# Kernel optimization log

Hardware: AMD Instinct MI355X
Metric: run time of the kernel (lower is better)

## Reference

```python
import jax, jax.numpy as jnp
import numpy as np

EPS = 1e-5

def ste_sign(x):
    # forward: sign(x) in {-1,+1}; backward: straight-through with |x|<=1 clip
    xc = jnp.clip(x, -1.0, 1.0)
    s = jnp.where(x >= 0, 1.0, -1.0).astype(x.dtype)
    return xc + jax.lax.stop_gradient(s - xc)

def quant_w(w):
    # 1-bit weight: sign(w) scaled by mean |w| (XNOR-Net style)
    return ste_sign(w) * jnp.mean(jnp.abs(w))

def qconv(x, w, stride, pad):
    # quantized conv: binarize activations and weights, then dense conv
    xq = ste_sign(x)
    wq = quant_w(w)
    return jax.lax.conv_general_dilated(
        xq, wq, window_strides=(stride, stride),
        padding=[(pad, pad), (pad, pad)],
        dimension_numbers=('NCHW', 'OIHW', 'NCHW'))

def batchnorm(x, gamma, beta):
    # training-mode BN: batch statistics over (N, H, W)
    mu = jnp.mean(x, axis=(0, 2, 3), keepdims=True)
    var = jnp.var(x, axis=(0, 2, 3), keepdims=True)
    xhat = (x - mu) * jax.lax.rsqrt(var + EPS)
    return xhat * gamma[None, :, None, None] + beta[None, :, None, None]

def setup_inputs() -> dict:
    key = jax.random.key(0)
    ks = jax.random.split(key, 4)
    in_planes, planes = 128, 256
    x = jax.random.normal(ks[0], (64, in_planes, 56, 56), dtype=jnp.float32)
    w1 = jax.random.normal(ks[1], (planes, in_planes, 3, 3), dtype=jnp.float32) * 0.05
    w2 = jax.random.normal(ks[2], (planes, planes, 3, 3), dtype=jnp.float32) * 0.05
    ws = jax.random.normal(ks[3], (planes, in_planes, 1, 1), dtype=jnp.float32) * 0.05
    g1 = jnp.ones((planes,), jnp.float32); b1 = jnp.zeros((planes,), jnp.float32)
    g2 = jnp.ones((planes,), jnp.float32); b2 = jnp.zeros((planes,), jnp.float32)
    return {'x': x, 'w1': w1, 'g1': g1, 'b1': b1, 'w2': w2, 'g2': g2, 'b2': b2, 'ws': ws}

def reference(x, w1, g1, b1, w2, g2, b2, ws):
    out = batchnorm(qconv(x, w1, stride=2, pad=1), g1, b1)   # [N,256,28,28]
    out = qconv(out, w2, stride=1, pad=1)
    out = out + qconv(x, ws, stride=2, pad=0)                # quantized 1x1 shortcut
    out = batchnorm(out, g2, b2)
    return out
```

## Files before the change

### kernel.cpp

```cpp
#include <hip/hip_runtime.h>
#include <stdint.h>

#define N_    64
#define CIN   128
#define CMID  256
#define H_    56
#define W_    56
#define OH    28
#define OW    28
#define NPIX  (OH*OW)
#define MPAD  800
#define MTOT  (N_*MPAD)
#define CNT_CH (N_*NPIX)
#define PXH   58
#define PYH   30
#define EPS_  1e-5f

#define STATS_BYTES 16384
#define OFF_PXI 16384
#define OFF_PYI (OFF_PXI + 27551744)
#define OFF_W1F (OFF_PYI + 14745600)
#define OFF_W2F (OFF_W1F + 294912)
#define OFF_WSF (OFF_W2F + 589824)
#define MEMSET_BYTES OFF_W1F

typedef int v4i  __attribute__((ext_vector_type(4)));
typedef int v16i __attribute__((ext_vector_type(16)));

#define MFMA_I8 __builtin_amdgcn_mfma_i32_32x32x32_i8

typedef const __attribute__((address_space(1))) void* gas_t;
typedef __attribute__((address_space(3))) void* las_t;

__device__ __forceinline__ void gl_lds16(const void* g, void* l) {
  __builtin_amdgcn_global_load_lds((gas_t)g, (las_t)l, 16, 0, 0);
}

__global__ __launch_bounds__(256) void reduce_abs_k(const float* __restrict__ w, int n,
                                                    float* __restrict__ out) {
  float s = 0.f;
  for (int i = blockIdx.x * 256 + threadIdx.x; i < n; i += gridDim.x * 256)
    s += fabsf(w[i]);
  for (int off = 32; off; off >>= 1) s += __shfl_down(s, off);
  if ((threadIdx.x & 63) == 0) atomicAdd(out, s);
}

__global__ __launch_bounds__(256) void pack_x_k(const float* __restrict__ x,
                                                int8_t* __restrict__ px) {
  int idx = blockIdx.x * 256 + threadIdx.x;
  int n = idx / (H_ * W_), hw = idx - n * (H_ * W_);
  int ih = hw / W_, iw = hw - ih * W_;
  const float* xp = x + ((size_t)n * CIN) * (H_ * W_) + hw;
  uint32_t wd[32];
#pragma unroll
  for (int c4 = 0; c4 < 32; ++c4) {
    uint32_t wv = 0u;
#pragma unroll
    for (int j = 0; j < 4; ++j) {
      uint32_t b = (xp[(size_t)(c4 * 4 + j) * (H_ * W_)] >= 0.f) ? 0x01u : 0xFFu;
      wv |= b << (j * 8);
    }
    wd[c4] = wv;
  }
  uint4* dst = (uint4*)(px + (((size_t)n * (PXH * PXH) + (ih + 1) * PXH + (iw + 1)) * CIN));
#pragma unroll
  for (int q = 0; q < 8; ++q)
    dst[q] = make_uint4(wd[q * 4], wd[q * 4 + 1], wd[q * 4 + 2], wd[q * 4 + 3]);
}

__global__ __launch_bounds__(256) void packw1f_k(const float* __restrict__ w1,
                                                 uint32_t* __restrict__ w1f) {
  int T = blockIdx.x * 256 + threadIdx.x;
  int l = T & 63, fb = T >> 6;
  int nb = fb & 7, kc = fb >> 3;
  int o = nb * 32 + (l & 31);
  int kbase = kc * 32 + (l >> 5) * 16;
  uint32_t wd[4] = {0u, 0u, 0u, 0u};
#pragma unroll
  for (int j = 0; j < 16; ++j) {
    int k = kbase + j, t = k >> 7, c = k & 127;
    uint32_t b = (w1[((size_t)o * CIN + c) * 9 + t] >= 0.f) ? 0x01u : 0xFFu;
    wd[j >> 2] |= b << ((j & 3) * 8);
  }
  ((uint4*)w1f)[T] = make_uint4(wd[0], wd[1], wd[2], wd[3]);
}

__global__ __launch_bounds__(256) void packw2f_k(const float* __restrict__ w2,
                                                 uint32_t* __restrict__ w2f) {
  int T = blockIdx.x * 256 + threadIdx.x;
  int l = T & 63, fb = T >> 6;
  int nb = fb & 7, kc = fb >> 3;
  int o = nb * 32 + (l & 31);
  int kbase = kc * 32 + (l >> 5) * 16;
  uint32_t wd[4] = {0u, 0u, 0u, 0u};
#pragma unroll
  for (int j = 0; j < 16; ++j) {
    int k = kbase + j, t = k >> 8, c = k & 255;
    uint32_t b = (w2[((size_t)o * CMID + c) * 9 + t] >= 0.f) ? 0x01u : 0xFFu;
    wd[j >> 2] |= b << ((j & 3) * 8);
  }
  ((uint4*)w2f)[T] = make_uint4(wd[0], wd[1], wd[2], wd[3]);
}

__global__ __launch_bounds__(256) void packwsf_k(const float* __restrict__ ws,
                                                 uint32_t* __restrict__ wsf) {
  int T = blockIdx.x * 256 + threadIdx.x;
  int l = T & 63, fb = T >> 6;
  int nb = fb & 7, kc = fb >> 3;
  int o = nb * 32 + (l & 31);
  int kbase = kc * 32 + (l >> 5) * 16;
  uint32_t wd[4] = {0u, 0u, 0u, 0u};
#pragma unroll
  for (int j = 0; j < 16; ++j) {
    int c = kbase + j;
    uint32_t b = (ws[(size_t)o * CIN + c] >= 0.f) ? 0x01u : 0xFFu;
    wd[j >> 2] |= b << ((j & 3) * 8);
  }
  ((uint4*)wsf)[T] = make_uint4(wd[0], wd[1], wd[2], wd[3]);
}

__global__ __launch_bounds__(256, 2) void conv1_k(const int8_t* __restrict__ px,
                                                  const uint8_t* __restrict__ w1f,
                                                  short* __restrict__ y16,
                                                  float* __restrict__ stats) {
  __shared__ int8_t lds[2][32768];
  int bid = (blockIdx.x & 7) * 100 + (blockIdx.x >> 3);
  int bnh = bid & 1, bm = bid >> 1;
  int tid = threadIdx.x, w = tid >> 6, l = tid & 63;
  int l31 = l & 31, lhi = l >> 5;
  int blockM = bm * 128;
  int waveM = blockM + (w & 1) * 64;
  int waveN = bnh * 128 + (w >> 1) * 64;
  int nbgl2 = (w >> 1) * 2;

  int srcsw = (((l & 7) ^ (l >> 3)) << 4);
  uint32_t rowoff[4];
#pragma unroll
  for (int i = 0; i < 4; ++i) {
    int p = blockM + (w * 4 + i) * 8 + (l >> 3);
    int n = p / MPAD, hw = p - n * MPAD;
    if (hw >= NPIX) hw = 0;
    int oh = hw / OW, ow = hw - oh * OW;
    rowoff[i] = (uint32_t)((n * (PXH * PXH) + (2 * oh) * PXH + 2 * ow) * CIN);
  }
  int sw = (l31 & 7) << 4;
  uint32_t aoff[2][4];
#pragma unroll
  for (int m = 0; m < 2; ++m) {
    int pxl = (w & 1) * 64 + m * 32 + l31;
#pragma unroll
    for (int kcl = 0; kcl < 4; ++kcl)
      aoff[m][kcl] = (uint32_t)(pxl * 128 + ((kcl * 32 + lhi * 16) ^ sw));
  }

  v16i acc[2][2] = {};

  auto stage = [&](int t, int8_t* buf) {
    int kh = t / 3, kw = t - 3 * kh;
    uint32_t tapoff = (uint32_t)((kh * PXH + kw) * CIN);
#pragma unroll
    for (int i = 0; i < 4; ++i) {
      int ch = w * 4 + i;
      gl_lds16(px + (size_t)(rowoff[i] + tapoff) + srcsw, buf + ch * 1024);
      gl_lds16(w1f + ((size_t)(((t * 4 + w) * 8) + bnh * 4 + i) << 10) + l * 16,
               buf + 16384 + ch * 1024);
    }
  };

  stage(0, lds[0]);
  __syncthreads();
  for (int it = 0; it < 9; ++it) {
    if (it < 8) stage(it + 1, lds[(it + 1) & 1]);
    const int8_t* cbuf = lds[it & 1];
    v4i a[2][4], b[2][4];
#pragma unroll
    for (int m = 0; m < 2; ++m)
#pragma unroll
      for (int kcl = 0; kcl < 4; ++kcl)
        a[m][kcl] = *(const v4i*)(cbuf + aoff[m][kcl]);
#pragma unroll
    for (int n2 = 0; n2 < 2; ++n2)
#pragma unroll
      for (int kcl = 0; kcl < 4; ++kcl)
        b[n2][kcl] = *(const v4i*)(cbuf + 16384 + (kcl * 4 + nbgl2 + n2) * 1024 + l * 16);
#pragma unroll
    for (int kcl = 0; kcl < 4; ++kcl) {
      acc[0][0] = MFMA_I8(a[0][kcl], b[0][kcl], acc[0][0], 0, 0, 0);
      acc[0][1] = MFMA_I8(a[0][kcl], b[1][kcl], acc[0][1], 0, 0, 0);
      acc[1][0] = MFMA_I8(a[1][kcl], b[0][kcl], acc[1][0], 0, 0, 0);
      acc[1][1] = MFMA_I8(a[1][kcl], b[1][kcl], acc[1][1], 0, 0, 0);
    }
    __syncthreads();
  }

#pragma unroll
  for (int n2 = 0; n2 < 2; ++n2) {
    int o = waveN + n2 * 32 + l31;
    float ssum = 0.f, ssq = 0.f;
#pragma unroll
    for (int m = 0; m < 2; ++m) {
      int tbase = waveM + m * 32;
      int nb0 = tbase / MPAD, r0 = tbase - nb0 * MPAD;
#pragma unroll
      for (int r = 0; r < 16; ++r) {
        int row = (r & 3) + 8 * (r >> 2) + 4 * lhi;
        int hwr = r0 + row;
        int d = acc[m][n2][r];
        bool valid = hwr < NPIX;
        if (valid) y16[((size_t)nb0 * NPIX + hwr) * CMID + o] = (short)d;
        float fd = valid ? (float)d : 0.f;
        ssum += fd; ssq += fd * fd;
      }
    }
    ssum += __shfl_down(ssum, 32);
    ssq  += __shfl_down(ssq, 32);
    if (l < 32) { atomicAdd(&stats[16 + o], ssum); atomicAdd(&stats[272 + o], ssq); }
  }
}

__global__ void bn1_prep_k(float* __restrict__ stats,
                           const float* __restrict__ g1,
                           const float* __restrict__ b1) {
  int c = threadIdx.x;
  float alpha1 = stats[0] * (1.f / (CMID * CIN * 9));
  float S = stats[16 + c], S2 = stats[272 + c];
  float mu = alpha1 * (S * (1.f / CNT_CH));
  float ey2 = alpha1 * alpha1 * (S2 * (1.f / CNT_CH));
  float var = fmaxf(ey2 - mu * mu, 0.f);
  float rs = rsqrtf(var + EPS_);
  float g = g1[c];
  stats[1552 + c] = g * rs * alpha1;
  stats[1808 + c] = b1[c] - g * rs * mu;
}

__global__ __launch_bounds__(256) void pack_y_k(const short* __restrict__ y16,
                                                const float* __restrict__ stats,
                                                int8_t* __restrict__ py) {
  int gid = blockIdx.x * 256 + threadIdx.x;
  int cg = gid & 31, pix = gid >> 5;
  int n = pix / NPIX, hw = pix - n * NPIX;
  int oh = hw / OW, ow = hw - oh * OW;
  uint4 raw = *(const uint4*)(y16 + (size_t)pix * CMID + cg * 8);
  const float* A = stats + 1552 + cg * 8;
  const float* B = stats + 1808 + cg * 8;
  float4 A0 = *(const float4*)A, A1 = *(const float4*)(A + 4);
  float4 B0 = *(const float4*)B, B1 = *(const float4*)(B + 4);
  int s[8];
  s[0] = (int)(short)(raw.x & 0xFFFF); s[1] = ((int)raw.x) >> 16;
  s[2] = (int)(short)(raw.y & 0xFFFF); s[3] = ((int)raw.y) >> 16;
  s[4] = (int)(short)(raw.z & 0xFFFF); s[5] = ((int)raw.z) >> 16;
  s[6] = (int)(short)(raw.w & 0xFFFF); s[7] = ((int)raw.w) >> 16;
  float a[8] = {A0.x, A0.y, A0.z, A0.w, A1.x, A1.y, A1.z, A1.w};
  float b[8] = {B0.x, B0.y, B0.z, B0.w, B1.x, B1.y, B1.z, B1.w};
  uint32_t w0 = 0u, w1 = 0u;
#pragma unroll
  for (int j = 0; j < 4; ++j) {
    w0 |= ((fmaf(a[j], (float)s[j], b[j]) >= 0.f) ? 0x01u : 0xFFu) << (j * 8);
    w1 |= ((fmaf(a[4 + j], (float)s[4 + j], b[4 + j]) >= 0.f) ? 0x01u : 0xFFu) << (j * 8);
  }
  size_t off = ((size_t)n * (PYH * PYH) + (oh + 1) * PYH + (ow + 1)) * CMID + cg * 8;
  *(uint2*)(py + off) = make_uint2(w0, w1);
}

__global__ __launch_bounds__(256, 2) void conv2_k(const int8_t* __restrict__ py,
                                                  const int8_t* __restrict__ px,
                                                  const uint8_t* __restrict__ w2f,
                                                  const uint8_t* __restrict__ wsf,
                                                  const float* __restrict__ stats,
                                                  float* __restrict__ out,
                                                  float* __restrict__ statw) {
  __shared__ int8_t lds[2][32768];
  int bid = (blockIdx.x & 7) * 100 + (blockIdx.x >> 3);
  int bnh = bid & 1, bm = bid >> 1;
  int tid = threadIdx.x, w = tid >> 6, l = tid & 63;
  int l31 = l & 31, lhi = l >> 5;
  int blockM = bm * 128;
  int waveM = blockM + (w & 1) * 64;
  int waveN = bnh * 128 + (w >> 1) * 64;
  int nbgl2 = (w >> 1) * 2;

  int srcsw = (((l & 7) ^ (l >> 3)) << 4);
  uint32_t rowoff[4], sxoff[4];
#pragma unroll
  for (int i = 0; i < 4; ++i) {
    int p = blockM + (w * 4 + i) * 8 + (l >> 3);
    int n = p / MPAD, hw = p - n * MPAD;
    if (hw >= NPIX) hw = 0;
    int oh = hw / OW, ow = hw - oh * OW;
    rowoff[i] = (uint32_t)((n * (PYH * PYH) + oh * PYH + ow) * CMID);
    sxoff[i]  = (uint32_t)((n * (PXH * PXH) + (2 * oh + 1) * PXH + (2 * ow + 1)) * CIN);
  }
  int sw = (l31 & 7) << 4;
  uint32_t aoff[2][4];
#pragma unroll
  for (int m = 0; m < 2; ++m) {
    int pxl = (w & 1) * 64 + m * 32 + l31;
#pragma unroll
    for (int kcl = 0; kcl < 4; ++kcl)
      aoff[m][kcl] = (uint32_t)(pxl * 128 + ((kcl * 32 + lhi * 16) ^ sw));
  }

  v16i am[2][2] = {};

  auto stageM = [&](int j, int8_t* buf) {
    int t = j >> 1, h = j & 1;
    int kh = t / 3, kw = t - 3 * kh;
    uint32_t tapoff = (uint32_t)((kh * PYH + kw) * CMID + h * 128);
    int kc = t * 8 + h * 4 + w;
#pragma unroll
    for (int i = 0; i < 4; ++i) {
      int ch = w * 4 + i;
      gl_lds16(py + (size_t)(rowoff[i] + tapoff) + srcsw, buf + ch * 1024);
      gl_lds16(w2f + ((size_t)(kc * 8 + bnh * 4 + i) << 10) + l * 16,
               buf + 16384 + ch * 1024);
    }
  };
  auto computeM = [&](const int8_t* cbuf, v16i (&ac)[2][2]) {
    v4i a[2][4], b[2][4];
#pragma unroll
    for (int m = 0; m < 2; ++m)
#pragma unroll
      for (int kcl = 0; kcl < 4; ++kcl)
        a[m][kcl] = *(const v4i*)(cbuf + aoff[m][kcl]);
#pragma unroll
    for (int n2 = 0; n2 < 2; ++n2)
#pragma unroll
      for (int kcl = 0; kcl < 4; ++kcl)
        b[n2][kcl] = *(const v4i*)(cbuf + 16384 + (kcl * 4 + nbgl2 + n2) * 1024 + l * 16);
#pragma unroll
    for (int kcl = 0; kcl < 4; ++kcl) {
      ac[0][0] = MFMA_I8(a[0][kcl], b[0][kcl], ac[0][0], 0, 0, 0);
      ac[0][1] = MFMA_I8(a[0][kcl], b[1][kcl], ac[0][1], 0, 0, 0);
      ac[1][0] = MFMA_I8(a[1][kcl], b[0][kcl], ac[1][0], 0, 0, 0);
      ac[1][1] = MFMA_I8(a[1][kcl], b[1][kcl], ac[1][1], 0, 0, 0);
    }
  };

  stageM(0, lds[0]);
  __syncthreads();
  for (int it = 0; it < 17; ++it) {
    stageM(it + 1, lds[(it + 1) & 1]);
    computeM(lds[it & 1], am);
    __syncthreads();
  }
  {
    int8_t* buf = lds[0];
#pragma unroll
    for (int i = 0; i < 4; ++i) {
      int ch = w * 4 + i;
      gl_lds16(px + (size_t)sxoff[i] + srcsw, buf + ch * 1024);
      gl_lds16(wsf + ((size_t)(w * 8 + bnh * 4 + i) << 10) + l * 16,
               buf + 16384 + ch * 1024);
    }
  }
  computeM(lds[1], am);
  __syncthreads();
  v16i as[2][2] = {};
  computeM(lds[0], as);

  float a2  = stats[1] * (1.f / (CMID * CMID * 9));
  float asx = stats[2] * (1.f / (CMID * CIN));
#pragma unroll
  for (int n2 = 0; n2 < 2; ++n2) {
    int o = waveN + n2 * 32 + l31;
    float ssum = 0.f, ssq = 0.f;
#pragma unroll
    for (int m = 0; m < 2; ++m) {
      int tbase = waveM + m * 32;
      int nb0 = tbase / MPAD, r0 = tbase - nb0 * MPAD;
#pragma unroll
      for (int r = 0; r < 16; ++r) {
        int row = (r & 3) + 8 * (r >> 2) + 4 * lhi;
        int hwr = r0 + row;
        bool valid = hwr < NPIX;
        float v = a2 * (float)am[m][n2][r] + asx * (float)as[m][n2][r];
        if (valid) out[((size_t)nb0 * CMID + o) * NPIX + hwr] = v;
        float vm = valid ? v : 0.f;
        ssum += vm; ssq += vm * vm;
      }
    }
    ssum += __shfl_down(ssum, 32);
    ssq  += __shfl_down(ssq, 32);
    if (l < 32) { atomicAdd(&statw[528 + o], ssum); atomicAdd(&statw[784 + o], ssq); }
  }
}

__global__ void bn2_prep_k(float* __restrict__ stats,
                           const float* __restrict__ g2,
                           const float* __restrict__ b2) {
  int c = threadIdx.x;
  float S = stats[528 + c], S2 = stats[784 + c];
  float mu = S * (1.f / CNT_CH);
  float var = fmaxf(S2 * (1.f / CNT_CH) - mu * mu, 0.f);
  float rs = rsqrtf(var + EPS_);
  float g = g2[c];
  stats[1040 + c] = g * rs;
  stats[1296 + c] = b2[c] - g * rs * mu;
}

__global__ __launch_bounds__(256) void bn2_apply_k(float4* __restrict__ out,
                                                   const float* __restrict__ stats) {
  int idx = blockIdx.x * 256 + threadIdx.x;
  int c = (idx / (NPIX / 4)) & (CMID - 1);
  float sc = stats[1040 + c], of = stats[1296 + c];
  float4 v = out[idx];
  v.x = v.x * sc + of; v.y = v.y * sc + of; v.z = v.z * sc + of; v.w = v.w * sc + of;
  out[idx] = v;
}

extern "C" void kernel_launch(void* const* d_in, const int* in_sizes, int n_in,
                              void* d_out, int out_size, void* d_ws, size_t ws_size,
                              hipStream_t stream) {
  const float* x   = (const float*)d_in[0];
  const float* w1  = (const float*)d_in[1];
  const float* g1  = (const float*)d_in[2];
  const float* b1  = (const float*)d_in[3];
  const float* w2  = (const float*)d_in[4];
  const float* g2  = (const float*)d_in[5];
  const float* b2  = (const float*)d_in[6];
  const float* wsc = (const float*)d_in[7];
  float* out = (float*)d_out;

  char* ws = (char*)d_ws;
  float*    stats = (float*)ws;
  int8_t*   pxi = (int8_t*)(ws + OFF_PXI);
  int8_t*   pyi = (int8_t*)(ws + OFF_PYI);
  uint32_t* w1f = (uint32_t*)(ws + OFF_W1F);
  uint32_t* w2f = (uint32_t*)(ws + OFF_W2F);
  uint32_t* wsf = (uint32_t*)(ws + OFF_WSF);
  short*    y16 = (short*)d_out;

  hipMemsetAsync(ws, 0, MEMSET_BYTES, stream);

  reduce_abs_k<<<128, 256, 0, stream>>>(w1,  CMID * CIN * 9,  &stats[0]);
  reduce_abs_k<<<256, 256, 0, stream>>>(w2,  CMID * CMID * 9, &stats[1]);
  reduce_abs_k<<<32,  256, 0, stream>>>(wsc, CMID * CIN,      &stats[2]);

  pack_x_k<<<784, 256, 0, stream>>>(x, pxi);
  packw1f_k<<<72, 256, 0, stream>>>(w1, w1f);
  packw2f_k<<<144, 256, 0, stream>>>(w2, w2f);
  packwsf_k<<<8, 256, 0, stream>>>(wsc, wsf);

  conv1_k<<<800, 256, 0, stream>>>(pxi, (const uint8_t*)w1f, y16, stats);
  bn1_prep_k<<<1, 256, 0, stream>>>(stats, g1, b1);
  pack_y_k<<<6272, 256, 0, stream>>>(y16, stats, pyi);
  conv2_k<<<800, 256, 0, stream>>>(pyi, pxi, (const uint8_t*)w2f, (const uint8_t*)wsf,
                                   stats, out, stats);
  bn2_prep_k<<<1, 256, 0, stream>>>(stats, g2, b2);
  bn2_apply_k<<<12544, 256, 0, stream>>>((float4*)out, stats);
}
```

Baseline: 362.9 us.

## Fuse weight abs-reduction into packing, zero only halos, fold BN prep kernels

```diff
diff --git a/kernel.cpp b/kernel.cpp
--- a/kernel.cpp
+++ b/kernel.cpp
@@ -22,7 +22,6 @@
 #define OFF_W1F (OFF_PYI + 14745600)
 #define OFF_W2F (OFF_W1F + 294912)
 #define OFF_WSF (OFF_W2F + 589824)
-#define MEMSET_BYTES OFF_W1F
 
 typedef int v4i  __attribute__((ext_vector_type(4)));
 typedef int v16i __attribute__((ext_vector_type(16)));
@@ -36,17 +35,20 @@
   __builtin_amdgcn_global_load_lds((gas_t)g, (las_t)l, 16, 0, 0);
 }
 
-__global__ __launch_bounds__(256) void reduce_abs_k(const float* __restrict__ w, int n,
-                                                    float* __restrict__ out) {
-  float s = 0.f;
-  for (int i = blockIdx.x * 256 + threadIdx.x; i < n; i += gridDim.x * 256)
-    s += fabsf(w[i]);
-  for (int off = 32; off; off >>= 1) s += __shfl_down(s, off);
-  if ((threadIdx.x & 63) == 0) atomicAdd(out, s);
-}
-
 __global__ __launch_bounds__(256) void pack_x_k(const float* __restrict__ x,
                                                 int8_t* __restrict__ px) {
+  if (blockIdx.x >= 784) {
+    int t = (blockIdx.x - 784) * 256 + threadIdx.x;
+    int q = t & 7, pp = t >> 3;
+    int n = pp / 228, p = pp - n * 228;
+    int ih, iw;
+    if (p < 58)        { ih = 0;  iw = p; }
+    else if (p < 116)  { ih = 57; iw = p - 58; }
+    else { int qq = p - 116; ih = 1 + (qq >> 1); iw = (qq & 1) * 57; }
+    uint4* dst = (uint4*)(px + ((size_t)n * (PXH * PXH) + ih * PXH + iw) * CIN);
+    dst[q] = make_uint4(0u, 0u, 0u, 0u);
+    return;
+  }
   int idx = blockIdx.x * 256 + threadIdx.x;
   int n = idx / (H_ * W_), hw = idx - n * (H_ * W_);
   int ih = hw / W_, iw = hw - ih * W_;
@@ -68,55 +70,67 @@
     dst[q] = make_uint4(wd[q * 4], wd[q * 4 + 1], wd[q * 4 + 2], wd[q * 4 + 3]);
 }
 
-__global__ __launch_bounds__(256) void packw1f_k(const float* __restrict__ w1,
-                                                 uint32_t* __restrict__ w1f) {
-  int T = blockIdx.x * 256 + threadIdx.x;
-  int l = T & 63, fb = T >> 6;
-  int nb = fb & 7, kc = fb >> 3;
-  int o = nb * 32 + (l & 31);
-  int kbase = kc * 32 + (l >> 5) * 16;
-  uint32_t wd[4] = {0u, 0u, 0u, 0u};
-#pragma unroll
-  for (int j = 0; j < 16; ++j) {
-    int k = kbase + j, t = k >> 7, c = k & 127;
-    uint32_t b = (w1[((size_t)o * CIN + c) * 9 + t] >= 0.f) ? 0x01u : 0xFFu;
-    wd[j >> 2] |= b << ((j & 3) * 8);
-  }
-  ((uint4*)w1f)[T] = make_uint4(wd[0], wd[1], wd[2], wd[3]);
-}
-
-__global__ __launch_bounds__(256) void packw2f_k(const float* __restrict__ w2,
-                                                 uint32_t* __restrict__ w2f) {
-  int T = blockIdx.x * 256 + threadIdx.x;
-  int l = T & 63, fb = T >> 6;
-  int nb = fb & 7, kc = fb >> 3;
-  int o = nb * 32 + (l & 31);
-  int kbase = kc * 32 + (l >> 5) * 16;
-  uint32_t wd[4] = {0u, 0u, 0u, 0u};
-#pragma unroll
-  for (int j = 0; j < 16; ++j) {
-    int k = kbase + j, t = k >> 8, c = k & 255;
-    uint32_t b = (w2[((size_t)o * CMID + c) * 9 + t] >= 0.f) ? 0x01u : 0xFFu;
-    wd[j >> 2] |= b << ((j & 3) * 8);
-  }
-  ((uint4*)w2f)[T] = make_uint4(wd[0], wd[1], wd[2], wd[3]);
-}
-
-__global__ __launch_bounds__(256) void packwsf_k(const float* __restrict__ ws,
-                                                 uint32_t* __restrict__ wsf) {
-  int T = blockIdx.x * 256 + threadIdx.x;
-  int l = T & 63, fb = T >> 6;
-  int nb = fb & 7, kc = fb >> 3;
-  int o = nb * 32 + (l & 31);
-  int kbase = kc * 32 + (l >> 5) * 16;
-  uint32_t wd[4] = {0u, 0u, 0u, 0u};
-#pragma unroll
-  for (int j = 0; j < 16; ++j) {
-    int c = kbase + j;
-    uint32_t b = (ws[(size_t)o * CIN + c] >= 0.f) ? 0x01u : 0xFFu;
-    wd[j >> 2] |= b << ((j & 3) * 8);
-  }
-  ((uint4*)wsf)[T] = make_uint4(wd[0], wd[1], wd[2], wd[3]);
+__global__ __launch_bounds__(256) void packw_all_k(const float* __restrict__ w1,
+                                                   const float* __restrict__ w2,
+                                                   const float* __restrict__ ws,
+                                                   uint32_t* __restrict__ w1f,
+                                                   uint32_t* __restrict__ w2f,
+                                                   uint32_t* __restrict__ wsf,
+                                                   float* __restrict__ stats) {
+  int bx = blockIdx.x;
+  float s = 0.f;
+  if (bx < 72) {
+    int T = bx * 256 + threadIdx.x;
+    int l = T & 63, fb = T >> 6;
+    int nb = fb & 7, kc = fb >> 3;
+    int o = nb * 32 + (l & 31);
+    int kbase = kc * 32 + (l >> 5) * 16;
+    uint32_t wd[4] = {0u, 0u, 0u, 0u};
+#pragma unroll
+    for (int j = 0; j < 16; ++j) {
+      int k = kbase + j, t = k >> 7, c = k & 127;
+      float wv = w1[((size_t)o * CIN + c) * 9 + t];
+      s += fabsf(wv);
+      wd[j >> 2] |= ((wv >= 0.f) ? 0x01u : 0xFFu) << ((j & 3) * 8);
+    }
+    ((uint4*)w1f)[T] = make_uint4(wd[0], wd[1], wd[2], wd[3]);
+    for (int off = 32; off; off >>= 1) s += __shfl_down(s, off);
+    if ((threadIdx.x & 63) == 0) atomicAdd(&stats[0], s);
+  } else if (bx < 216) {
+    int T = (bx - 72) * 256 + threadIdx.x;
+    int l = T & 63, fb = T >> 6;
+    int nb = fb & 7, kc = fb >> 3;
+    int o = nb * 32 + (l & 31);
+    int kbase = kc * 32 + (l >> 5) * 16;
+    uint32_t wd[4] = {0u, 0u, 0u, 0u};
+#pragma unroll
+    for (int j = 0; j < 16; ++j) {
+      int k = kbase + j, t = k >> 8, c = k & 255;
+      float wv = w2[((size_t)o * CMID + c) * 9 + t];
+      s += fabsf(wv);
+      wd[j >> 2] |= ((wv >= 0.f) ? 0x01u : 0xFFu) << ((j & 3) * 8);
+    }
+    ((uint4*)w2f)[T] = make_uint4(wd[0], wd[1], wd[2], wd[3]);
+    for (int off = 32; off; off >>= 1) s += __shfl_down(s, off);
+    if ((threadIdx.x & 63) == 0) atomicAdd(&stats[1], s);
+  } else {
+    int T = (bx - 216) * 256 + threadIdx.x;
+    int l = T & 63, fb = T >> 6;
+    int nb = fb & 7, kc = fb >> 3;
+    int o = nb * 32 + (l & 31);
+    int kbase = kc * 32 + (l >> 5) * 16;
+    uint32_t wd[4] = {0u, 0u, 0u, 0u};
+#pragma unroll
+    for (int j = 0; j < 16; ++j) {
+      int c = kbase + j;
+      float wv = ws[(size_t)o * CIN + c];
+      s += fabsf(wv);
+      wd[j >> 2] |= ((wv >= 0.f) ? 0x01u : 0xFFu) << ((j & 3) * 8);
+    }
+    ((uint4*)wsf)[T] = make_uint4(wd[0], wd[1], wd[2], wd[3]);
+    for (int off = 32; off; off >>= 1) s += __shfl_down(s, off);
+    if ((threadIdx.x & 63) == 0) atomicAdd(&stats[2], s);
+  }
 }
 
 __global__ __launch_bounds__(256, 2) void conv1_k(const int8_t* __restrict__ px,
@@ -218,40 +232,47 @@
   }
 }
 
-__global__ void bn1_prep_k(float* __restrict__ stats,
-                           const float* __restrict__ g1,
-                           const float* __restrict__ b1) {
-  int c = threadIdx.x;
-  float alpha1 = stats[0] * (1.f / (CMID * CIN * 9));
-  float S = stats[16 + c], S2 = stats[272 + c];
-  float mu = alpha1 * (S * (1.f / CNT_CH));
-  float ey2 = alpha1 * alpha1 * (S2 * (1.f / CNT_CH));
-  float var = fmaxf(ey2 - mu * mu, 0.f);
-  float rs = rsqrtf(var + EPS_);
-  float g = g1[c];
-  stats[1552 + c] = g * rs * alpha1;
-  stats[1808 + c] = b1[c] - g * rs * mu;
-}
-
 __global__ __launch_bounds__(256) void pack_y_k(const short* __restrict__ y16,
                                                 const float* __restrict__ stats,
+                                                const float* __restrict__ g1,
+                                                const float* __restrict__ b1,
                                                 int8_t* __restrict__ py) {
+  if (blockIdx.x >= 6272) {
+    int t = (blockIdx.x - 6272) * 256 + threadIdx.x;
+    int q = t & 15, pp = t >> 4;
+    int n = pp / 116, p = pp - n * 116;
+    int ih, iw;
+    if (p < 30)       { ih = 0;  iw = p; }
+    else if (p < 60)  { ih = 29; iw = p - 30; }
+    else { int qq = p - 60; ih = 1 + (qq >> 1); iw = (qq & 1) * 29; }
+    uint4* dst = (uint4*)(py + ((size_t)n * (PYH * PYH) + ih * PYH + iw) * CMID);
+    dst[q] = make_uint4(0u, 0u, 0u, 0u);
+    return;
+  }
   int gid = blockIdx.x * 256 + threadIdx.x;
   int cg = gid & 31, pix = gid >> 5;
   int n = pix / NPIX, hw = pix - n * NPIX;
   int oh = hw / OW, ow = hw - oh * OW;
   uint4 raw = *(const uint4*)(y16 + (size_t)pix * CMID + cg * 8);
-  const float* A = stats + 1552 + cg * 8;
-  const float* B = stats + 1808 + cg * 8;
-  float4 A0 = *(const float4*)A, A1 = *(const float4*)(A + 4);
-  float4 B0 = *(const float4*)B, B1 = *(const float4*)(B + 4);
+  float alpha1 = stats[0] * (1.f / (CMID * CIN * 9));
+  float a[8], b[8];
+#pragma unroll
+  for (int j = 0; j < 8; ++j) {
+    int c = cg * 8 + j;
+    float S = stats[16 + c], S2 = stats[272 + c];
+    float mu = alpha1 * (S * (1.f / CNT_CH));
+    float ey2 = alpha1 * alpha1 * (S2 * (1.f / CNT_CH));
+    float var = fmaxf(ey2 - mu * mu, 0.f);
+    float rs = rsqrtf(var + EPS_);
+    float g = g1[c];
+    a[j] = g * rs * alpha1;
+    b[j] = b1[c] - g * rs * mu;
+  }
   int s[8];
   s[0] = (int)(short)(raw.x & 0xFFFF); s[1] = ((int)raw.x) >> 16;
   s[2] = (int)(short)(raw.y & 0xFFFF); s[3] = ((int)raw.y) >> 16;
   s[4] = (int)(short)(raw.z & 0xFFFF); s[5] = ((int)raw.z) >> 16;
   s[6] = (int)(short)(raw.w & 0xFFFF); s[7] = ((int)raw.w) >> 16;
-  float a[8] = {A0.x, A0.y, A0.z, A0.w, A1.x, A1.y, A1.z, A1.w};
-  float b[8] = {B0.x, B0.y, B0.z, B0.w, B1.x, B1.y, B1.z, B1.w};
   uint32_t w0 = 0u, w1 = 0u;
 #pragma unroll
   for (int j = 0; j < 4; ++j) {
@@ -385,24 +406,18 @@
   }
 }
 
-__global__ void bn2_prep_k(float* __restrict__ stats,
-                           const float* __restrict__ g2,
-                           const float* __restrict__ b2) {
-  int c = threadIdx.x;
+__global__ __launch_bounds__(256) void bn2_apply_k(float4* __restrict__ out,
+                                                   const float* __restrict__ stats,
+                                                   const float* __restrict__ g2,
+                                                   const float* __restrict__ b2) {
+  int idx = blockIdx.x * 256 + threadIdx.x;
+  int c = (idx / (NPIX / 4)) & (CMID - 1);
   float S = stats[528 + c], S2 = stats[784 + c];
   float mu = S * (1.f / CNT_CH);
   float var = fmaxf(S2 * (1.f / CNT_CH) - mu * mu, 0.f);
   float rs = rsqrtf(var + EPS_);
   float g = g2[c];
-  stats[1040 + c] = g * rs;
-  stats[1296 + c] = b2[c] - g * rs * mu;
-}
-
-__global__ __launch_bounds__(256) void bn2_apply_k(float4* __restrict__ out,
-                                                   const float* __restrict__ stats) {
-  int idx = blockIdx.x * 256 + threadIdx.x;
-  int c = (idx / (NPIX / 4)) & (CMID - 1);
-  float sc = stats[1040 + c], of = stats[1296 + c];
+  float sc = g * rs, of = b2[c] - g * rs * mu;
   float4 v = out[idx];
   v.x = v.x * sc + of; v.y = v.y * sc + of; v.z = v.z * sc + of; v.w = v.w * sc + of;
   out[idx] = v;
@@ -430,22 +445,14 @@
   uint32_t* wsf = (uint32_t*)(ws + OFF_WSF);
   short*    y16 = (short*)d_out;
 
-  hipMemsetAsync(ws, 0, MEMSET_BYTES, stream);
-
-  reduce_abs_k<<<128, 256, 0, stream>>>(w1,  CMID * CIN * 9,  &stats[0]);
-  reduce_abs_k<<<256, 256, 0, stream>>>(w2,  CMID * CMID * 9, &stats[1]);
-  reduce_abs_k<<<32,  256, 0, stream>>>(wsc, CMID * CIN,      &stats[2]);
-
-  pack_x_k<<<784, 256, 0, stream>>>(x, pxi);
-  packw1f_k<<<72, 256, 0, stream>>>(w1, w1f);
-  packw2f_k<<<144, 256, 0, stream>>>(w2, w2f);
-  packwsf_k<<<8, 256, 0, stream>>>(wsc, wsf);
+  hipMemsetAsync(ws, 0, STATS_BYTES, stream);
+
+  pack_x_k<<<1240, 256, 0, stream>>>(x, pxi);
+  packw_all_k<<<224, 256, 0, stream>>>(w1, w2, wsc, w1f, w2f, wsf, stats);
 
   conv1_k<<<800, 256, 0, stream>>>(pxi, (const uint8_t*)w1f, y16, stats);
-  bn1_prep_k<<<1, 256, 0, stream>>>(stats, g1, b1);
-  pack_y_k<<<6272, 256, 0, stream>>>(y16, stats, pyi);
+  pack_y_k<<<6736, 256, 0, stream>>>(y16, stats, g1, b1, pyi);
   conv2_k<<<800, 256, 0, stream>>>(pyi, pxi, (const uint8_t*)w2f, (const uint8_t*)wsf,
                                    stats, out, stats);
-  bn2_prep_k<<<1, 256, 0, stream>>>(stats, g2, b2);
-  bn2_apply_k<<<12544, 256, 0, stream>>>((float4*)out, stats);
-}
+  bn2_apply_k<<<12544, 256, 0, stream>>>((float4*)out, stats, g2, b2);
+}
```

Result: faster. 340.2 us (-6.3%).
